# Kernel tuning notes

Measured on AMD Instinct MI355X. Metric: run time of the kernel, lower is better.

Reference implementation:

```python
import jax, jax.numpy as jnp
import numpy as np

N = 100000
E = 1600000
IN_DIM = 256
HID = 128
LAYERS = 8
ALPHA = 0.1
THETA = 0.5


def setup_inputs() -> dict:
    key = jax.random.key(0)
    ks = jax.random.split(key, 6)
    x = jax.random.normal(ks[0], (N, IN_DIM), dtype=jnp.float32)
    edge_index = jax.random.randint(ks[1], (2, E), 0, N, dtype=jnp.int64)
    W_in = jax.random.normal(ks[2], (IN_DIM, HID), dtype=jnp.float32) / np.sqrt(IN_DIM)
    b_in = jnp.zeros((HID,), dtype=jnp.float32)
    convs_W = jax.random.normal(ks[3], (LAYERS, HID, HID), dtype=jnp.float32) / np.sqrt(HID)
    W_out = jax.random.normal(ks[4], (HID, 1), dtype=jnp.float32) / np.sqrt(HID)
    b_out = jnp.zeros((1,), dtype=jnp.float32)
    return {"x": x, "edge_index": edge_index, "W_in": W_in, "b_in": b_in,
            "convs_W": convs_W, "W_out": W_out, "b_out": b_out}


def reference(x, edge_index, W_in, b_in, convs_W, W_out, b_out):
    row = edge_index[0]  # source nodes
    col = edge_index[1]  # destination nodes
    # gcn_norm with self-loops: deg = in-degree + 1
    deg = jax.ops.segment_sum(jnp.ones((E,), dtype=jnp.float32), col, num_segments=N) + 1.0
    dinv = jax.lax.rsqrt(deg)
    norm = dinv[row] * dinv[col]            # [E] edge weights
    self_norm = dinv * dinv                 # [N] self-loop weights (1/deg)

    def propagate(h):
        # Ahat @ h : gather-scale-scatter over edges + self-loop term
        msgs = h[row] * norm[:, None]       # [E, HID]
        return jax.ops.segment_sum(msgs, col, num_segments=N) + h * self_norm[:, None]

    h0 = jax.nn.relu(x @ W_in + b_in)       # initial residual
    h = h0
    for i in range(LAYERS):
        agg = propagate(h)
        s = (1.0 - ALPHA) * agg + ALPHA * h0
        beta = float(np.log(THETA / (i + 1) + 1.0))
        h = jax.nn.relu((1.0 - beta) * s + beta * (s @ convs_W[i]))
    return (h @ W_out + b_out).squeeze(-1)  # [N]
```

## Files before the change

kernel.cpp:

```cpp
#include <hip/hip_runtime.h>
#include <math.h>

#define HID 128
#define NB 32
#define SBST 136
#define XST 264
#define CSH 9
#define MCH 8192
#define GOFF (32 * SBST)

typedef unsigned int uint32;
typedef unsigned short ushort_t;
typedef __attribute__((ext_vector_type(8))) short bf16x8;
typedef __attribute__((ext_vector_type(4))) float f32x4;

__device__ __forceinline__ unsigned short f2bf(float f) {
    unsigned u = __float_as_uint(f);
    u += 0x7FFF + ((u >> 16) & 1);
    return (unsigned short)(u >> 16);
}
__device__ __forceinline__ float bf_lo(uint32 u) { return __uint_as_float(u << 16); }
__device__ __forceinline__ float bf_hi(uint32 u) { return __uint_as_float(u & 0xFFFF0000u); }

__global__ void degree_k(const int* __restrict__ col, int* __restrict__ counts, int E) {
    int e = blockIdx.x * 256 + threadIdx.x;
    if (e < E) atomicAdd(&counts[col[e]], 1);
}

__global__ void scan1_k(const int* __restrict__ counts, int* __restrict__ row_ptr,
                        int* __restrict__ blocksums, float* __restrict__ dinv, int N) {
    __shared__ int tmp[256];
    int t = threadIdx.x;
    int i = blockIdx.x * 256 + t;
    int v = (i < N) ? counts[i] : 0;
    if (i < N) dinv[i] = rsqrtf((float)v + 1.0f);
    tmp[t] = v;
    __syncthreads();
    for (int off = 1; off < 256; off <<= 1) {
        int x = (t >= off) ? tmp[t - off] : 0;
        __syncthreads();
        tmp[t] += x;
        __syncthreads();
    }
    if (i < N) row_ptr[i] = tmp[t] - v;
    if (t == 255) blocksums[blockIdx.x] = tmp[t];
}

__global__ void scan2_k(const int* __restrict__ blocksums, int* __restrict__ blockoffs, int nb) {
    __shared__ int tmp[512];
    int t = threadIdx.x;
    int v = (t < nb) ? blocksums[t] : 0;
    tmp[t] = v;
    __syncthreads();
    for (int off = 1; off < 512; off <<= 1) {
        int x = (t >= off) ? tmp[t - off] : 0;
        __syncthreads();
        tmp[t] += x;
        __syncthreads();
    }
    if (t < nb) blockoffs[t] = tmp[t] - v;
}

__global__ void scan3_k(int* __restrict__ row_ptr, int* __restrict__ cursor,
                        int* __restrict__ ccursor,
                        const int* __restrict__ blockoffs, int N, int E) {
    int i = blockIdx.x * 256 + threadIdx.x;
    if (i < N) {
        int v = row_ptr[i] + blockoffs[blockIdx.x];
        row_ptr[i] = v;
        cursor[i] = v;
        if ((i & ((1 << CSH) - 1)) == 0) ccursor[i >> CSH] = v;
    }
    if (i == 0) row_ptr[N] = E;
}

__global__ __launch_bounds__(256) void multisplit_k(const int* __restrict__ row,
                                                    const int* __restrict__ col,
                                                    int* __restrict__ ccursor,
                                                    int2* __restrict__ ebuf,
                                                    int E, int NCO) {
    __shared__ int lcnt[256];
    __shared__ int gbase[256];
    __shared__ int lpos[256];
    int t = threadIdx.x;
    int e0 = blockIdx.x * MCH;
    lcnt[t] = 0;
    lpos[t] = 0;
    __syncthreads();
    for (int i = t; i < MCH; i += 256) {
        int e = e0 + i;
        if (e < E) atomicAdd(&lcnt[col[e] >> CSH], 1);
    }
    __syncthreads();
    if (t < NCO && lcnt[t] > 0) gbase[t] = atomicAdd(&ccursor[t], lcnt[t]);
    __syncthreads();
    for (int i = t; i < MCH; i += 256) {
        int e = e0 + i;
        if (e < E) {
            int c = col[e];
            int b = c >> CSH;
            int p = atomicAdd(&lpos[b], 1);
            ebuf[gbase[b] + p] = make_int2(row[e], c);
        }
    }
}

__global__ void cfinal_k(const int2* __restrict__ ebuf, const int* __restrict__ row_ptr,
                         int* __restrict__ cursor, int* __restrict__ srcS, int N) {
    int b = blockIdx.x;
    int n0 = b << CSH;
    int n1 = n0 + (1 << CSH);
    if (n1 > N) n1 = N;
    int beg = row_ptr[n0];
    int end = row_ptr[n1];
    for (int i = beg + threadIdx.x; i < end; i += 256) {
        int2 p = ebuf[i];
        int pos = atomicAdd(&cursor[p.y], 1);
        srcS[pos] = p.x;
    }
}

__global__ void wprep_k(const float* __restrict__ convs, short* __restrict__ Wt) {
    int idx = blockIdx.x * 256 + threadIdx.x;
    if (idx >= 8 * 128 * 128) return;
    int l = idx >> 14;
    int r = idx & 16383;
    int k = r >> 7;
    int n = r & 127;
    Wt[(l << 14) + (n << 7) + k] = (short)f2bf(convs[idx]);
}

__global__ void winprep_k(const float* __restrict__ Win, short* __restrict__ Winb) {
    int idx = blockIdx.x * 256 + threadIdx.x;
    if (idx >= 256 * 128) return;
    int k = idx >> 7;
    int n = idx & 127;
    Winb[n * 256 + k] = (short)f2bf(Win[idx]);
}

__global__ __launch_bounds__(256) void h0_k(const float* __restrict__ x,
                                            const short* __restrict__ Winb,
                                            const float* __restrict__ bin,
                                            const float* __restrict__ dinv,
                                            ushort_t* __restrict__ h0b,
                                            ushort_t* __restrict__ g,
                                            int N) {
    __shared__ short xs[GOFF + 32 * SBST];
    __shared__ float s_dv[NB];
    int t = threadIdx.x;
    int base = blockIdx.x * NB;

    if (t < NB) s_dv[t] = (base + t < N) ? dinv[base + t] : 1.f;

    for (int idx = t; idx < NB * 64; idx += 256) {
        int m = idx >> 6;
        int kk = (idx & 63) * 4;
        int nn = base + m;
        float4 v = make_float4(0.f, 0.f, 0.f, 0.f);
        if (nn < N) v = *(const float4*)&x[(size_t)nn * 256 + kk];
        uint2 pk;
        pk.x = ((uint32)f2bf(v.y) << 16) | (uint32)f2bf(v.x);
        pk.y = ((uint32)f2bf(v.w) << 16) | (uint32)f2bf(v.z);
        *(uint2*)&xs[m * XST + kk] = pk;
    }
    __syncthreads();

    int lane = t & 63, wv = t >> 6;
    int mt = (wv & 1) * 16;
    int jb = wv >> 1;
    int lrow = lane & 15;
    int lq = lane >> 4;
    f32x4 acc0 = {0.f, 0.f, 0.f, 0.f};
    f32x4 acc1 = {0.f, 0.f, 0.f, 0.f};
    f32x4 acc2 = {0.f, 0.f, 0.f, 0.f};
    f32x4 acc3 = {0.f, 0.f, 0.f, 0.f};
#pragma unroll
    for (int ks = 0; ks < 8; ks++) {
        bf16x8 a = *(const bf16x8*)&xs[(mt + lrow) * XST + ks * 32 + lq * 8];
        bf16x8 b0 = *(const bf16x8*)&Winb[((jb + 0) * 16 + lrow) * 256 + ks * 32 + lq * 8];
        bf16x8 b1 = *(const bf16x8*)&Winb[((jb + 2) * 16 + lrow) * 256 + ks * 32 + lq * 8];
        bf16x8 b2 = *(const bf16x8*)&Winb[((jb + 4) * 16 + lrow) * 256 + ks * 32 + lq * 8];
        bf16x8 b3 = *(const bf16x8*)&Winb[((jb + 6) * 16 + lrow) * 256 + ks * 32 + lq * 8];
        acc0 = __builtin_amdgcn_mfma_f32_16x16x32_bf16(a, b0, acc0, 0, 0, 0);
        acc1 = __builtin_amdgcn_mfma_f32_16x16x32_bf16(a, b1, acc1, 0, 0, 0);
        acc2 = __builtin_amdgcn_mfma_f32_16x16x32_bf16(a, b2, acc2, 0, 0, 0);
        acc3 = __builtin_amdgcn_mfma_f32_16x16x32_bf16(a, b3, acc3, 0, 0, 0);
    }

    __syncthreads();
#pragma unroll
    for (int q = 0; q < 4; q++) {
        f32x4 accq = (q == 0) ? acc0 : (q == 1) ? acc1 : (q == 2) ? acc2 : acc3;
        int j0 = (jb + 2 * q) * 16;
        float bj = bin[j0 + lrow];
#pragma unroll
        for (int r = 0; r < 4; r++) {
            int rowm = mt + lq * 4 + r;
            float h = fmaxf(accq[r] + bj, 0.f);
            xs[rowm * SBST + j0 + lrow] = (short)f2bf(h);
            xs[GOFF + rowm * SBST + j0 + lrow] = (short)f2bf(s_dv[rowm] * h);
        }
    }
    __syncthreads();
    for (int idx = t; idx < NB * 16; idx += 256) {
        int rowm = idx >> 4;
        int c = (idx & 15) * 8;
        int dst = base + rowm;
        if (dst < N) {
            *(bf16x8*)&h0b[(size_t)dst * HID + c] = *(const bf16x8*)&xs[rowm * SBST + c];
            *(bf16x8*)&g[(size_t)dst * HID + c]   = *(const bf16x8*)&xs[GOFF + rowm * SBST + c];
        }
    }
}

__global__ __launch_bounds__(256) void layer_k(const ushort_t* __restrict__ g_in,
                                               ushort_t* __restrict__ g_out,
                                               const ushort_t* __restrict__ h0b,
                                               const float* __restrict__ dinv,
                                               const int* __restrict__ row_ptr,
                                               const int* __restrict__ srcS,
                                               const short* __restrict__ Wtb,
                                               float beta, int N) {
    __shared__ float s_f32[NB * HID];
    __shared__ short s_bf[NB * SBST];
    __shared__ float s_dv[NB];
    int t = threadIdx.x;
    int lane = t & 63;
    int wv = t >> 6;
    int base = blockIdx.x * NB;

    if (t < NB) s_dv[t] = dinv[base + t];

    const char* gbp = (const char*)g_in;
    uint32 lb = (uint32)(lane << 2);
    for (int m = wv; m < NB; m += 4) {
        int dst = base + m;
        if (dst >= N) {
            s_f32[m * HID + lane * 2] = 0.f;
            s_f32[m * HID + lane * 2 + 1] = 0.f;
            *(uint32*)&s_bf[m * SBST + lane * 2] = 0;
            continue;
        }
        float dv = dinv[dst];
        uint32 gd = ((const uint32*)(g_in + (size_t)dst * HID))[lane];
        uint32 hu = ((const uint32*)(h0b + (size_t)dst * HID))[lane];
        float ax = bf_lo(gd), ay = bf_hi(gd);
        int beg = __builtin_amdgcn_readfirstlane(row_ptr[dst]);
        int end = __builtin_amdgcn_readfirstlane(row_ptr[dst + 1]);
        for (int e = beg; e < end; e += 16) {
            int rem = end - e;
            int ii = e + (lane & 15);
            if (ii > end - 1) ii = end - 1;
            int sv = srcS[ii];
            int s0  = __builtin_amdgcn_readlane(sv, 0);
            int s1  = __builtin_amdgcn_readlane(sv, 1);
            int s2  = __builtin_amdgcn_readlane(sv, 2);
            int s3  = __builtin_amdgcn_readlane(sv, 3);
            int s4  = __builtin_amdgcn_readlane(sv, 4);
            int s5  = __builtin_amdgcn_readlane(sv, 5);
            int s6  = __builtin_amdgcn_readlane(sv, 6);
            int s7  = __builtin_amdgcn_readlane(sv, 7);
            int s8  = __builtin_amdgcn_readlane(sv, 8);
            int s9  = __builtin_amdgcn_readlane(sv, 9);
            int s10 = __builtin_amdgcn_readlane(sv, 10);
            int s11 = __builtin_amdgcn_readlane(sv, 11);
            int s12 = __builtin_amdgcn_readlane(sv, 12);
            int s13 = __builtin_amdgcn_readlane(sv, 13);
            int s14 = __builtin_amdgcn_readlane(sv, 14);
            int s15 = __builtin_amdgcn_readlane(sv, 15);
            uint32 g0  = *(const uint32*)(gbp + (((uint32)s0  << 8) | lb));
            uint32 g1  = *(const uint32*)(gbp + (((uint32)s1  << 8) | lb));
            uint32 g2  = *(const uint32*)(gbp + (((uint32)s2  << 8) | lb));
            uint32 g3  = *(const uint32*)(gbp + (((uint32)s3  << 8) | lb));
            uint32 g4  = *(const uint32*)(gbp + (((uint32)s4  << 8) | lb));
            uint32 g5  = *(const uint32*)(gbp + (((uint32)s5  << 8) | lb));
            uint32 g6  = *(const uint32*)(gbp + (((uint32)s6  << 8) | lb));
            uint32 g7  = *(const uint32*)(gbp + (((uint32)s7  << 8) | lb));
            uint32 g8  = *(const uint32*)(gbp + (((uint32)s8  << 8) | lb));
            uint32 g9  = *(const uint32*)(gbp + (((uint32)s9  << 8) | lb));
            uint32 g10 = *(const uint32*)(gbp + (((uint32)s10 << 8) | lb));
            uint32 g11 = *(const uint32*)(gbp + (((uint32)s11 << 8) | lb));
            uint32 g12 = *(const uint32*)(gbp + (((uint32)s12 << 8) | lb));
            uint32 g13 = *(const uint32*)(gbp + (((uint32)s13 << 8) | lb));
            uint32 g14 = *(const uint32*)(gbp + (((uint32)s14 << 8) | lb));
            uint32 g15 = *(const uint32*)(gbp + (((uint32)s15 << 8) | lb));
            ax += bf_lo(g0); ay += bf_hi(g0);
            if (rem > 1)  { ax += bf_lo(g1);  ay += bf_hi(g1);  }
            if (rem > 2)  { ax += bf_lo(g2);  ay += bf_hi(g2);  }
            if (rem > 3)  { ax += bf_lo(g3);  ay += bf_hi(g3);  }
            if (rem > 4)  { ax += bf_lo(g4);  ay += bf_hi(g4);  }
            if (rem > 5)  { ax += bf_lo(g5);  ay += bf_hi(g5);  }
            if (rem > 6)  { ax += bf_lo(g6);  ay += bf_hi(g6);  }
            if (rem > 7)  { ax += bf_lo(g7);  ay += bf_hi(g7);  }
            if (rem > 8)  { ax += bf_lo(g8);  ay += bf_hi(g8);  }
            if (rem > 9)  { ax += bf_lo(g9);  ay += bf_hi(g9);  }
            if (rem > 10) { ax += bf_lo(g10); ay += bf_hi(g10); }
            if (rem > 11) { ax += bf_lo(g11); ay += bf_hi(g11); }
            if (rem > 12) { ax += bf_lo(g12); ay += bf_hi(g12); }
            if (rem > 13) { ax += bf_lo(g13); ay += bf_hi(g13); }
            if (rem > 14) { ax += bf_lo(g14); ay += bf_hi(g14); }
            if (rem > 15) { ax += bf_lo(g15); ay += bf_hi(g15); }
        }
        float sc = 0.9f * dv;
        float sx = sc * ax + 0.1f * bf_lo(hu);
        float sy = sc * ay + 0.1f * bf_hi(hu);
        s_f32[m * HID + lane * 2]     = sx;
        s_f32[m * HID + lane * 2 + 1] = sy;
        uint32 pk = ((uint32)f2bf(sy) << 16) | (uint32)f2bf(sx);
        *(uint32*)&s_bf[m * SBST + lane * 2] = pk;
    }
    __syncthreads();

    int mt = (wv & 1) * 16;
    int jb = wv >> 1;
    int lrow = lane & 15;
    int lq = lane >> 4;
    f32x4 acc0 = {0.f, 0.f, 0.f, 0.f};
    f32x4 acc1 = {0.f, 0.f, 0.f, 0.f};
    f32x4 acc2 = {0.f, 0.f, 0.f, 0.f};
    f32x4 acc3 = {0.f, 0.f, 0.f, 0.f};
#pragma unroll
    for (int ks = 0; ks < 4; ks++) {
        bf16x8 a = *(const bf16x8*)&s_bf[(mt + lrow) * SBST + ks * 32 + lq * 8];
        bf16x8 b0 = *(const bf16x8*)&Wtb[((jb + 0) * 16 + lrow) * 128 + ks * 32 + lq * 8];
        bf16x8 b1 = *(const bf16x8*)&Wtb[((jb + 2) * 16 + lrow) * 128 + ks * 32 + lq * 8];
        bf16x8 b2 = *(const bf16x8*)&Wtb[((jb + 4) * 16 + lrow) * 128 + ks * 32 + lq * 8];
        bf16x8 b3 = *(const bf16x8*)&Wtb[((jb + 6) * 16 + lrow) * 128 + ks * 32 + lq * 8];
        acc0 = __builtin_amdgcn_mfma_f32_16x16x32_bf16(a, b0, acc0, 0, 0, 0);
        acc1 = __builtin_amdgcn_mfma_f32_16x16x32_bf16(a, b1, acc1, 0, 0, 0);
        acc2 = __builtin_amdgcn_mfma_f32_16x16x32_bf16(a, b2, acc2, 0, 0, 0);
        acc3 = __builtin_amdgcn_mfma_f32_16x16x32_bf16(a, b3, acc3, 0, 0, 0);
    }

    __syncthreads();
    float ob = 1.0f - beta;
#pragma unroll
    for (int q = 0; q < 4; q++) {
        f32x4 accq = (q == 0) ? acc0 : (q == 1) ? acc1 : (q == 2) ? acc2 : acc3;
        int j0 = (jb + 2 * q) * 16;
#pragma unroll
        for (int r = 0; r < 4; r++) {
            int rowm = mt + lq * 4 + r;
            float sv = s_f32[rowm * HID + j0 + lrow];
            float h = fmaxf(ob * sv + beta * accq[r], 0.f);
            s_bf[rowm * SBST + j0 + lrow] = (short)f2bf(s_dv[rowm] * h);
        }
    }
    __syncthreads();
    for (int idx = t; idx < NB * 16; idx += 256) {
        int rowm = idx >> 4;
        int c = (idx & 15) * 8;
        int dst = base + rowm;
        if (dst < N)
            *(bf16x8*)&g_out[(size_t)dst * HID + c] = *(const bf16x8*)&s_bf[rowm * SBST + c];
    }
}

__global__ void out_k(const ushort_t* __restrict__ g, const float* __restrict__ dinv,
                      const float* __restrict__ Wout, const float* __restrict__ bout,
                      float* __restrict__ out, int N) {
    int t = threadIdx.x;
    int lane = t & 63;
    int wv = t >> 6;
    int n = blockIdx.x * 4 + wv;
    if (n >= N) return;
    uint32 u = ((const uint32*)(g + (size_t)n * HID))[lane];
    float v = bf_lo(u) * Wout[lane * 2] + bf_hi(u) * Wout[lane * 2 + 1];
#pragma unroll
    for (int off = 32; off > 0; off >>= 1) v += __shfl_down(v, off, 64);
    if (lane == 0) out[n] = v / dinv[n] + bout[0];
}

extern "C" void kernel_launch(void* const* d_in, const int* in_sizes, int n_in,
                              void* d_out, int out_size, void* d_ws, size_t ws_size,
                              hipStream_t stream) {
    const float* x    = (const float*)d_in[0];
    const int*   ei   = (const int*)d_in[1];
    const float* Win  = (const float*)d_in[2];
    const float* bin  = (const float*)d_in[3];
    const float* convs= (const float*)d_in[4];
    const float* Wout = (const float*)d_in[5];
    const float* bout = (const float*)d_in[6];

    int N = in_sizes[0] / 256;
    int E = in_sizes[1] / 2;
    const int* row = ei;
    const int* col = ei + E;

    char* ws = (char*)d_ws;
    size_t off = 0;
    auto alloc = [&](size_t bytes) -> char* {
        char* p = ws + off;
        off = (off + bytes + 255) & ~(size_t)255;
        return p;
    };
    int NCO = (N + (1 << CSH) - 1) >> CSH;
    int*      counts    = (int*)alloc((size_t)N * 4);
    int*      row_ptr   = (int*)alloc((size_t)(N + 1) * 4);
    int*      cursor    = (int*)alloc((size_t)N * 4);
    int*      ccursor   = (int*)alloc((size_t)NCO * 4);
    int*      blocksums = (int*)alloc(512 * 4);
    int*      blockoffs = (int*)alloc(512 * 4);
    float*    dinv      = (float*)alloc((size_t)N * 4);
    int*      srcS      = (int*)alloc((size_t)E * 4);
    short*    Wt        = (short*)alloc((size_t)8 * 128 * 128 * 2);
    short*    Winb      = (short*)alloc((size_t)256 * 128 * 2);
    ushort_t* h0b       = (ushort_t*)alloc((size_t)N * HID * 2);
    ushort_t* gA        = (ushort_t*)alloc((size_t)N * HID * 2);
    ushort_t* gB        = (ushort_t*)alloc((size_t)N * HID * 2);
    int2*     ebuf      = (int2*)gB;

    int eb = (E + 255) / 256;
    int nb = (N + 255) / 256;
    int mb = (E + MCH - 1) / MCH;

    hipMemsetAsync(counts, 0, (size_t)N * 4, stream);
    degree_k<<<eb, 256, 0, stream>>>(col, counts, E);
    scan1_k<<<nb, 256, 0, stream>>>(counts, row_ptr, blocksums, dinv, N);
    scan2_k<<<1, 512, 0, stream>>>(blocksums, blockoffs, nb);
    scan3_k<<<nb, 256, 0, stream>>>(row_ptr, cursor, ccursor, blockoffs, N, E);
    multisplit_k<<<mb, 256, 0, stream>>>(row, col, ccursor, ebuf, E, NCO);
    cfinal_k<<<NCO, 256, 0, stream>>>(ebuf, row_ptr, cursor, srcS, N);
    wprep_k<<<512, 256, 0, stream>>>(convs, Wt);
    winprep_k<<<128, 256, 0, stream>>>(Win, Winb);

    int gb = (N + NB - 1) / NB;
    h0_k<<<gb, 256, 0, stream>>>(x, Winb, bin, dinv, h0b, gA, N);

    ushort_t* gin = gA;
    ushort_t* gout = gB;
    for (int i = 0; i < 8; i++) {
        float beta = (float)log(0.5 / (double)(i + 1) + 1.0);
        layer_k<<<gb, 256, 0, stream>>>(gin, gout, h0b, dinv, row_ptr, srcS,
                                        Wt + (size_t)i * 128 * 128, beta, N);
        ushort_t* tp = gin; gin = gout; gout = tp;
    }
    out_k<<<(N + 3) / 4, 256, 0, stream>>>(gin, dinv, Wout, bout, (float*)d_out, N);
}
```

Measured before the change: 1.078 ms.

## Fold residual blend into weights and stage block edge indices in LDS

Rewrites each layer weight as beta*W + (1-beta)*I, so the matmul yields the blended output directly and the fp32 shared copy of s is dropped. Each block now loads its contiguous range of neighbour indices into shared memory once, replacing the per-chunk readlane broadcasts from global memory, and falls back to direct global reads when a block has more than CAP edges. Launch bounds request 6 blocks per CU to raise occupancy now that LDS use is smaller. The folded identity term is rounded to bf16 together with W, which may cost a little accuracy.

```diff
diff --git a/kernel.cpp b/kernel.cpp
--- a/kernel.cpp
+++ b/kernel.cpp
@@ -8,6 +8,7 @@
 #define CSH 9
 #define MCH 8192
 #define GOFF (32 * SBST)
+#define CAP 1024
 
 typedef unsigned int uint32;
 typedef unsigned short ushort_t;
@@ -127,7 +128,9 @@
     int r = idx & 16383;
     int k = r >> 7;
     int n = r & 127;
-    Wt[(l << 14) + (n << 7) + k] = (short)f2bf(convs[idx]);
+    float beta = logf(0.5f / (float)(l + 1) + 1.0f);
+    float v = beta * convs[idx] + ((k == n) ? (1.0f - beta) : 0.0f);
+    Wt[(l << 14) + (n << 7) + k] = (short)f2bf(v);
 }
 
 __global__ void winprep_k(const float* __restrict__ Win, short* __restrict__ Winb) {
@@ -213,15 +216,16 @@
     }
 }
 
-__global__ __launch_bounds__(256) void layer_k(const ushort_t* __restrict__ g_in,
-                                               ushort_t* __restrict__ g_out,
-                                               const ushort_t* __restrict__ h0b,
-                                               const float* __restrict__ dinv,
-                                               const int* __restrict__ row_ptr,
-                                               const int* __restrict__ srcS,
-                                               const short* __restrict__ Wtb,
-                                               float beta, int N) {
-    __shared__ float s_f32[NB * HID];
+__global__ __launch_bounds__(256, 6) void layer_k(const ushort_t* __restrict__ g_in,
+                                                  ushort_t* __restrict__ g_out,
+                                                  const ushort_t* __restrict__ h0b,
+                                                  const float* __restrict__ dinv,
+                                                  const int* __restrict__ row_ptr,
+                                                  const int* __restrict__ srcS,
+                                                  const short* __restrict__ Wtb,
+                                                  int N) {
+    __shared__ int   s_idx[CAP + 16];
+    __shared__ int   s_rp[NB + 1];
     __shared__ short s_bf[NB * SBST];
     __shared__ float s_dv[NB];
     int t = threadIdx.x;
@@ -229,83 +233,100 @@
     int wv = t >> 6;
     int base = blockIdx.x * NB;
 
-    if (t < NB) s_dv[t] = dinv[base + t];
+    if (t < NB + 1) s_rp[t] = row_ptr[min(base + t, N)];
+    if (t < NB) s_dv[t] = (base + t < N) ? dinv[base + t] : 1.f;
+    int blk_beg = row_ptr[base];
+    int blk_end = row_ptr[min(base + NB, N)];
+    int nE = blk_end - blk_beg;
+    int nL = nE < CAP ? nE : CAP;
+    for (int i = t; i < nL; i += 256) s_idx[i] = srcS[blk_beg + i];
+    if (t < 16) s_idx[nL + t] = 0;
+    __syncthreads();
 
     const char* gbp = (const char*)g_in;
     uint32 lb = (uint32)(lane << 2);
     for (int m = wv; m < NB; m += 4) {
         int dst = base + m;
         if (dst >= N) {
-            s_f32[m * HID + lane * 2] = 0.f;
-            s_f32[m * HID + lane * 2 + 1] = 0.f;
             *(uint32*)&s_bf[m * SBST + lane * 2] = 0;
             continue;
         }
-        float dv = dinv[dst];
+        float dv = s_dv[m];
         uint32 gd = ((const uint32*)(g_in + (size_t)dst * HID))[lane];
         uint32 hu = ((const uint32*)(h0b + (size_t)dst * HID))[lane];
         float ax = bf_lo(gd), ay = bf_hi(gd);
-        int beg = __builtin_amdgcn_readfirstlane(row_ptr[dst]);
-        int end = __builtin_amdgcn_readfirstlane(row_ptr[dst + 1]);
-        for (int e = beg; e < end; e += 16) {
-            int rem = end - e;
-            int ii = e + (lane & 15);
-            if (ii > end - 1) ii = end - 1;
-            int sv = srcS[ii];
-            int s0  = __builtin_amdgcn_readlane(sv, 0);
-            int s1  = __builtin_amdgcn_readlane(sv, 1);
-            int s2  = __builtin_amdgcn_readlane(sv, 2);
-            int s3  = __builtin_amdgcn_readlane(sv, 3);
-            int s4  = __builtin_amdgcn_readlane(sv, 4);
-            int s5  = __builtin_amdgcn_readlane(sv, 5);
-            int s6  = __builtin_amdgcn_readlane(sv, 6);
-            int s7  = __builtin_amdgcn_readlane(sv, 7);
-            int s8  = __builtin_amdgcn_readlane(sv, 8);
-            int s9  = __builtin_amdgcn_readlane(sv, 9);
-            int s10 = __builtin_amdgcn_readlane(sv, 10);
-            int s11 = __builtin_amdgcn_readlane(sv, 11);
-            int s12 = __builtin_amdgcn_readlane(sv, 12);
-            int s13 = __builtin_amdgcn_readlane(sv, 13);
-            int s14 = __builtin_amdgcn_readlane(sv, 14);
-            int s15 = __builtin_amdgcn_readlane(sv, 15);
-            uint32 g0  = *(const uint32*)(gbp + (((uint32)s0  << 8) | lb));
-            uint32 g1  = *(const uint32*)(gbp + (((uint32)s1  << 8) | lb));
-            uint32 g2  = *(const uint32*)(gbp + (((uint32)s2  << 8) | lb));
-            uint32 g3  = *(const uint32*)(gbp + (((uint32)s3  << 8) | lb));
-            uint32 g4  = *(const uint32*)(gbp + (((uint32)s4  << 8) | lb));
-            uint32 g5  = *(const uint32*)(gbp + (((uint32)s5  << 8) | lb));
-            uint32 g6  = *(const uint32*)(gbp + (((uint32)s6  << 8) | lb));
-            uint32 g7  = *(const uint32*)(gbp + (((uint32)s7  << 8) | lb));
-            uint32 g8  = *(const uint32*)(gbp + (((uint32)s8  << 8) | lb));
-            uint32 g9  = *(const uint32*)(gbp + (((uint32)s9  << 8) | lb));
-            uint32 g10 = *(const uint32*)(gbp + (((uint32)s10 << 8) | lb));
-            uint32 g11 = *(const uint32*)(gbp + (((uint32)s11 << 8) | lb));
-            uint32 g12 = *(const uint32*)(gbp + (((uint32)s12 << 8) | lb));
-            uint32 g13 = *(const uint32*)(gbp + (((uint32)s13 << 8) | lb));
-            uint32 g14 = *(const uint32*)(gbp + (((uint32)s14 << 8) | lb));
-            uint32 g15 = *(const uint32*)(gbp + (((uint32)s15 << 8) | lb));
-            ax += bf_lo(g0); ay += bf_hi(g0);
-            if (rem > 1)  { ax += bf_lo(g1);  ay += bf_hi(g1);  }
-            if (rem > 2)  { ax += bf_lo(g2);  ay += bf_hi(g2);  }
-            if (rem > 3)  { ax += bf_lo(g3);  ay += bf_hi(g3);  }
-            if (rem > 4)  { ax += bf_lo(g4);  ay += bf_hi(g4);  }
-            if (rem > 5)  { ax += bf_lo(g5);  ay += bf_hi(g5);  }
-            if (rem > 6)  { ax += bf_lo(g6);  ay += bf_hi(g6);  }
-            if (rem > 7)  { ax += bf_lo(g7);  ay += bf_hi(g7);  }
-            if (rem > 8)  { ax += bf_lo(g8);  ay += bf_hi(g8);  }
-            if (rem > 9)  { ax += bf_lo(g9);  ay += bf_hi(g9);  }
-            if (rem > 10) { ax += bf_lo(g10); ay += bf_hi(g10); }
-            if (rem > 11) { ax += bf_lo(g11); ay += bf_hi(g11); }
-            if (rem > 12) { ax += bf_lo(g12); ay += bf_hi(g12); }
-            if (rem > 13) { ax += bf_lo(g13); ay += bf_hi(g13); }
-            if (rem > 14) { ax += bf_lo(g14); ay += bf_hi(g14); }
-            if (rem > 15) { ax += bf_lo(g15); ay += bf_hi(g15); }
+        int beg = s_rp[m], end = s_rp[m + 1];
+        int lend = end - blk_beg;
+        if (lend <= CAP) {
+            for (int e = beg - blk_beg; e < lend; e += 16) {
+                int rem = lend - e;
+                int i0  = s_idx[e + 0];
+                int i1  = s_idx[e + 1];
+                int i2  = s_idx[e + 2];
+                int i3  = s_idx[e + 3];
+                int i4  = s_idx[e + 4];
+                int i5  = s_idx[e + 5];
+                int i6  = s_idx[e + 6];
+                int i7  = s_idx[e + 7];
+                int i8  = s_idx[e + 8];
+                int i9  = s_idx[e + 9];
+                int i10 = s_idx[e + 10];
+                int i11 = s_idx[e + 11];
+                int i12 = s_idx[e + 12];
+                int i13 = s_idx[e + 13];
+                int i14 = s_idx[e + 14];
+                int i15 = s_idx[e + 15];
+                uint32 g0  = *(const uint32*)(gbp + (((uint32)i0  << 8) | lb));
+                uint32 g1  = *(const uint32*)(gbp + (((uint32)i1  << 8) | lb));
+                uint32 g2  = *(const uint32*)(gbp + (((uint32)i2  << 8) | lb));
+                uint32 g3  = *(const uint32*)(gbp + (((uint32)i3  << 8) | lb));
+                uint32 g4  = *(const uint32*)(gbp + (((uint32)i4  << 8) | lb));
+                uint32 g5  = *(const uint32*)(gbp + (((uint32)i5  << 8) | lb));
+                uint32 g6  = *(const uint32*)(gbp + (((uint32)i6  << 8) | lb));
+                uint32 g7  = *(const uint32*)(gbp + (((uint32)i7  << 8) | lb));
+                uint32 g8  = *(const uint32*)(gbp + (((uint32)i8  << 8) | lb));
+                uint32 g9  = *(const uint32*)(gbp + (((uint32)i9  << 8) | lb));
+                uint32 g10 = *(const uint32*)(gbp + (((uint32)i10 << 8) | lb));
+                uint32 g11 = *(const uint32*)(gbp + (((uint32)i11 << 8) | lb));
+                uint32 g12 = *(const uint32*)(gbp + (((uint32)i12 << 8) | lb));
+                uint32 g13 = *(const uint32*)(gbp + (((uint32)i13 << 8) | lb));
+                uint32 g14 = *(const uint32*)(gbp + (((uint32)i14 << 8) | lb));
+                uint32 g15 = *(const uint32*)(gbp + (((uint32)i15 << 8) | lb));
+                ax += bf_lo(g0); ay += bf_hi(g0);
+                if (rem > 1)  { ax += bf_lo(g1);  ay += bf_hi(g1);  }
+                if (rem > 2)  { ax += bf_lo(g2);  ay += bf_hi(g2);  }
+                if (rem > 3)  { ax += bf_lo(g3);  ay += bf_hi(g3);  }
+                if (rem > 4)  { ax += bf_lo(g4);  ay += bf_hi(g4);  }
+                if (rem > 5)  { ax += bf_lo(g5);  ay += bf_hi(g5);  }
+                if (rem > 6)  { ax += bf_lo(g6);  ay += bf_hi(g6);  }
+                if (rem > 7)  { ax += bf_lo(g7);  ay += bf_hi(g7);  }
+                if (rem > 8)  { ax += bf_lo(g8);  ay += bf_hi(g8);  }
+                if (rem > 9)  { ax += bf_lo(g9);  ay += bf_hi(g9);  }
+                if (rem > 10) { ax += bf_lo(g10); ay += bf_hi(g10); }
+                if (rem > 11) { ax += bf_lo(g11); ay += bf_hi(g11); }
+                if (rem > 12) { ax += bf_lo(g12); ay += bf_hi(g12); }
+                if (rem > 13) { ax += bf_lo(g13); ay += bf_hi(g13); }
+                if (rem > 14) { ax += bf_lo(g14); ay += bf_hi(g14); }
+                if (rem > 15) { ax += bf_lo(g15); ay += bf_hi(g15); }
+            }
+        } else {
+            for (int e = beg; e < end; e += 16) {
+                int rem = end - e;
+                int last = end - 1;
+#pragma unroll
+                for (int k = 0; k < 16; k++) {
+                    if (k < rem) {
+                        int ii = e + k;
+                        int sn = srcS[ii > last ? last : ii];
+                        uint32 gg = *(const uint32*)(gbp + (((uint32)sn << 8) | lb));
+                        ax += bf_lo(gg); ay += bf_hi(gg);
+                    }
+                }
+            }
         }
         float sc = 0.9f * dv;
         float sx = sc * ax + 0.1f * bf_lo(hu);
         float sy = sc * ay + 0.1f * bf_hi(hu);
-        s_f32[m * HID + lane * 2]     = sx;
-        s_f32[m * HID + lane * 2 + 1] = sy;
         uint32 pk = ((uint32)f2bf(sy) << 16) | (uint32)f2bf(sx);
         *(uint32*)&s_bf[m * SBST + lane * 2] = pk;
     }
@@ -333,7 +354,6 @@
     }
 
     __syncthreads();
-    float ob = 1.0f - beta;
 #pragma unroll
     for (int q = 0; q < 4; q++) {
         f32x4 accq = (q == 0) ? acc0 : (q == 1) ? acc1 : (q == 2) ? acc2 : acc3;
@@ -341,8 +361,7 @@
 #pragma unroll
         for (int r = 0; r < 4; r++) {
             int rowm = mt + lq * 4 + r;
-            float sv = s_f32[rowm * HID + j0 + lrow];
-            float h = fmaxf(ob * sv + beta * accq[r], 0.f);
+            float h = fmaxf(accq[r], 0.f);
             s_bf[rowm * SBST + j0 + lrow] = (short)f2bf(s_dv[rowm] * h);
         }
     }
@@ -430,9 +449,8 @@
     ushort_t* gin = gA;
     ushort_t* gout = gB;
     for (int i = 0; i < 8; i++) {
-        float beta = (float)log(0.5 / (double)(i + 1) + 1.0);
         layer_k<<<gb, 256, 0, stream>>>(gin, gout, h0b, dinv, row_ptr, srcS,
-                                        Wt + (size_t)i * 128 * 128, beta, N);
+                                        Wt + (size_t)i * 128 * 128, N);
         ushort_t* tp = gin; gin = gout; gout = tp;
     }
     out_k<<<(N + 3) / 4, 256, 0, stream>>>(gin, dinv, Wout, bout, (float*)d_out, N);
```

Measured after the change: 1.007 ms. 6.6% less time.
